# Performance work log

Measured on AMD Instinct MI355X. Metric: run time of the kernel, lower is better.

Reference implementation:

```python
import jax, jax.numpy as jnp
import numpy as np

DIM = 512
HEADS = 8
DIM_HEAD = 64
SCALE = DIM_HEAD ** -0.5


def setup_inputs() -> dict:
    key = jax.random.key(0)
    ks = jax.random.split(key, 4)
    b, n = 4, 2048
    x = jax.random.normal(ks[0], (b, n, DIM), dtype=jnp.float32)
    Wq = jax.random.normal(ks[1], (DIM, HEADS * DIM_HEAD), dtype=jnp.float32) * (DIM ** -0.5)
    Wkv = jax.random.normal(ks[2], (DIM, 2 * HEADS * DIM_HEAD), dtype=jnp.float32) * (DIM ** -0.5)
    Wo = jax.random.normal(ks[3], (HEADS * DIM_HEAD, DIM), dtype=jnp.float32) * ((HEADS * DIM_HEAD) ** -0.5)
    bo = jnp.zeros((DIM,), dtype=jnp.float32)
    return {"x": x, "Wq": Wq, "Wkv": Wkv, "Wo": Wo, "bo": bo}


def reference(x, Wq, Wkv, Wo, bo):
    b, n, _ = x.shape
    # context = x (self-attention path, kv_include_self=False)
    q = x @ Wq                      # [b, n, h*d]
    kv = x @ Wkv                    # [b, n, 2*h*d]
    k, v = jnp.split(kv, 2, axis=-1)

    def split_heads(t):
        return t.reshape(b, n, HEADS, DIM_HEAD).transpose(0, 2, 1, 3)  # [b,h,n,d]

    q, k, v = split_heads(q), split_heads(k), split_heads(v)
    dots = jnp.einsum('bhid,bhjd->bhij', q, k) * SCALE  # [b,h,n,n]
    attn = jax.nn.softmax(dots, axis=-1)
    out = jnp.einsum('bhij,bhjd->bhid', attn, v)        # [b,h,n,d]
    out = out.transpose(0, 2, 1, 3).reshape(b, n, HEADS * DIM_HEAD)
    return out @ Wo + bo
```

## Files before the change

### kernel.cpp

```cpp
#include <hip/hip_runtime.h>
#include <hip/hip_bf16.h>

typedef short bf16x8 __attribute__((ext_vector_type(8)));
typedef float fx4    __attribute__((ext_vector_type(4)));

#if __has_builtin(__builtin_amdgcn_exp2f)
#define EXP2 __builtin_amdgcn_exp2f
#else
#define EXP2 exp2f
#endif

__device__ __forceinline__ unsigned pk2(float a, float b) {
  union { __hip_bfloat162 h; unsigned u; } cv;
  cv.h = __float22bfloat162_rn(float2{a, b});
  return cv.u;
}
__device__ __forceinline__ uint2 pk4(const fx4& v) {
  uint2 r;
  r.x = pk2(v[0], v[1]);
  r.y = pk2(v[2], v[3]);
  return r;
}

__device__ __forceinline__ void gld16(const void* g, void* l) {
  __builtin_amdgcn_global_load_lds(
      (const __attribute__((address_space(1))) unsigned int*)g,
      (__attribute__((address_space(3))) unsigned int*)l, 16, 0, 0);
}

__device__ __forceinline__ void bar_raw() {
  asm volatile("s_barrier" ::: "memory");
}
__device__ __forceinline__ void bar_lgkm() {
  asm volatile("s_waitcnt lgkmcnt(0)\ns_barrier" ::: "memory");
}
__device__ __forceinline__ void bar_lgkm_vm4() {
  asm volatile("s_waitcnt vmcnt(4) lgkmcnt(0)\ns_barrier" ::: "memory");
}
__device__ __forceinline__ void cfence() { asm volatile("" ::: "memory"); }

__global__ __launch_bounds__(256) void prep_kernel(
    const float* __restrict__ x, const float* __restrict__ Wq,
    const float* __restrict__ Wkv, const float* __restrict__ Wo,
    short* __restrict__ xb, short* __restrict__ WallT, short* __restrict__ WoT,
    float qscale) {
  const int bx = blockIdx.x, tid = threadIdx.x;
  if (bx < 4096) {
    int i = bx * 256 + tid;
    const float4 s = *(const float4*)(x + (size_t)i * 4);
    uint2 o; o.x = pk2(s.x, s.y); o.y = pk2(s.z, s.w);
    *(uint2*)(xb + (size_t)i * 4) = o;
    return;
  }
  __shared__ float t[32][33];
  const int idx = bx - 4096;
  const int wb = idx & 63, kt = (idx >> 6) * 32;
  const bool mode0 = wb < 48;
  const int ct = (mode0 ? wb : wb - 48) * 32;
  const int tx = tid & 31, ty = tid >> 5;
  short* outT = mode0 ? WallT : WoT;
#pragma unroll
  for (int s = 0; s < 4; ++s) {
    int k = kt + ty + s * 8;
    int c = ct + tx;
    float v;
    if (mode0) v = (c < 512) ? Wq[(size_t)k * 512 + c] * qscale
                             : Wkv[(size_t)k * 1024 + (c - 512)];
    else       v = Wo[(size_t)k * 512 + c];
    t[ty + s * 8][tx] = v;
  }
  __syncthreads();
#pragma unroll
  for (int s = 0; s < 4; ++s) {
    int c = ct + ty + s * 8;
    int k = kt + tx;
    unsigned u = __float_as_uint(t[tx][ty + s * 8]);
    u = (u + 0x7fffu + ((u >> 16) & 1u)) >> 16;
    outT[(size_t)c * 512 + k] = (short)u;
  }
}

__global__ __launch_bounds__(256) void gemm_qkv(
    const short* __restrict__ A, const short* __restrict__ Bt,
    short* __restrict__ oq, short* __restrict__ ok, short* __restrict__ ovT) {
  __shared__ short As[2 * 128 * 32];
  __shared__ short Bs[2 * 128 * 32];
  const int K = 512;
  const int tid = threadIdx.x;
  const int wave = tid >> 6, lane = tid & 63;
  const int quad = lane >> 4, l15 = lane & 15;
  const int wm = wave >> 1, wn = wave & 1;
  const int m0 = blockIdx.y * 128, n0 = blockIdx.x * 128;
  const bool swapped = (n0 < 1024);

  int arow[4], aoff[4];
#pragma unroll
  for (int c = 0; c < 4; ++c) {
    int u = c * 256 + tid;
    int slab = u >> 9, r2 = u & 511;
    arow[c] = r2 >> 2;
    aoff[c] = slab * 32 + (r2 & 3) * 8;
  }

  fx4 acc[4][4];
#pragma unroll
  for (int i = 0; i < 4; ++i)
#pragma unroll
    for (int j = 0; j < 4; ++j) acc[i][j] = fx4{0.f, 0.f, 0.f, 0.f};

  bf16x8 apre[4];
#pragma unroll
  for (int c = 0; c < 4; ++c)
    apre[c] = *(const bf16x8*)(A + (size_t)(m0 + arow[c]) * K + aoff[c]);

  for (int k0 = 0; k0 < K; k0 += 64) {
    bar_raw();
#pragma unroll
    for (int c = 0; c < 4; ++c)
      *(bf16x8*)(As + (size_t)(c * 256 + tid) * 8) = apre[c];
#pragma unroll
    for (int c = 0; c < 4; ++c) {
      int u = c * 256 + tid;
      int slab = u >> 9, r2 = u & 511;
      gld16(Bt + (size_t)(n0 + (r2 >> 2)) * K + k0 + slab * 32 + (r2 & 3) * 8,
            Bs + (size_t)(c * 256 + wave * 64) * 8);
    }
    cfence();
    {
      int kn = (k0 + 64) & 511;
#pragma unroll
      for (int c = 0; c < 4; ++c)
        apre[c] = *(const bf16x8*)(A + (size_t)(m0 + arow[c]) * K + kn + aoff[c]);
    }
    bar_lgkm_vm4();

#pragma unroll
    for (int ks2 = 0; ks2 < 2; ++ks2) {
      bf16x8 af[4], bfr[4];
#pragma unroll
      for (int i = 0; i < 4; ++i)
        af[i] = *(const bf16x8*)(As + ks2 * 4096 + (wm * 64 + i * 16 + l15) * 32 + quad * 8);
#pragma unroll
      for (int i = 0; i < 4; ++i)
        bfr[i] = *(const bf16x8*)(Bs + ks2 * 4096 + (wn * 64 + i * 16 + l15) * 32 + quad * 8);
      if (swapped) {
#pragma unroll
        for (int mi = 0; mi < 4; ++mi)
#pragma unroll
          for (int ni = 0; ni < 4; ++ni)
            acc[mi][ni] = __builtin_amdgcn_mfma_f32_16x16x32_bf16(bfr[ni], af[mi], acc[mi][ni], 0, 0, 0);
      } else {
#pragma unroll
        for (int mi = 0; mi < 4; ++mi)
#pragma unroll
          for (int ni = 0; ni < 4; ++ni)
            acc[mi][ni] = __builtin_amdgcn_mfma_f32_16x16x32_bf16(af[mi], bfr[ni], acc[mi][ni], 0, 0, 0);
      }
    }
  }

  const int rowb = m0 + wm * 64;
  const int colb = n0 + wn * 64;
  const int cls = n0 >> 9;
  if (cls < 2) {
    short* base = (cls == 0) ? oq : ok;
#pragma unroll
    for (int mi = 0; mi < 4; ++mi) {
      int t = rowb + mi * 16 + l15;
      int bb = t >> 11, ii = t & 2047;
#pragma unroll
      for (int ni = 0; ni < 4; ++ni) {
        int f = (colb + ni * 16 + quad * 4) & 511;
        int hh = f >> 6, dd = f & 63;
        *(uint2*)(base + ((size_t)(bb * 8 + hh) * 2048 + ii) * 64 + dd) = pk4(acc[mi][ni]);
      }
    }
  } else {
#pragma unroll
    for (int mi = 0; mi < 4; ++mi) {
      int rbase = rowb + mi * 16 + quad * 4;
      int bb = rbase >> 11;
      int ii = rbase & 2047;
#pragma unroll
      for (int ni = 0; ni < 4; ++ni) {
        int c = (colb + ni * 16 + l15) & 511;
        int hh = c >> 6, dd = c & 63;
        *(uint2*)(ovT + ((size_t)(bb * 8 + hh) * 64 + dd) * 2048 + ii) = pk4(acc[mi][ni]);
      }
    }
  }
}

__global__ __launch_bounds__(256) void gemm_out(
    const short* __restrict__ A, const short* __restrict__ Bt,
    float* __restrict__ of, const float* __restrict__ bias) {
  __shared__ short As[2 * 64 * 32];
  __shared__ short Bs[2 * 128 * 32];
  const int K = 512, N = 512;
  const int tid = threadIdx.x;
  const int wave = tid >> 6, lane = tid & 63;
  const int quad = lane >> 4, l15 = lane & 15;
  const int wm = wave >> 1, wn = wave & 1;
  const int m0 = blockIdx.y * 64, n0 = blockIdx.x * 128;

  int arow[2], aoff[2], brow[4], boff[4];
#pragma unroll
  for (int c = 0; c < 2; ++c) {
    int u = c * 256 + tid;
    int slab = u >> 8, r2 = u & 255;
    arow[c] = r2 >> 2; aoff[c] = slab * 32 + (r2 & 3) * 8;
  }
#pragma unroll
  for (int c = 0; c < 4; ++c) {
    int u = c * 256 + tid;
    int slab = u >> 9, r2 = u & 511;
    brow[c] = r2 >> 2; boff[c] = slab * 32 + (r2 & 3) * 8;
  }

  fx4 acc[2][4];
#pragma unroll
  for (int i = 0; i < 2; ++i)
#pragma unroll
    for (int j = 0; j < 4; ++j) acc[i][j] = fx4{0.f, 0.f, 0.f, 0.f};

  bf16x8 apre[2], bpre[4];
#pragma unroll
  for (int c = 0; c < 2; ++c)
    apre[c] = *(const bf16x8*)(A + (size_t)(m0 + arow[c]) * K + aoff[c]);
#pragma unroll
  for (int c = 0; c < 4; ++c)
    bpre[c] = *(const bf16x8*)(Bt + (size_t)(n0 + brow[c]) * K + boff[c]);

  for (int k0 = 0; k0 < K; k0 += 64) {
    bar_raw();
#pragma unroll
    for (int c = 0; c < 2; ++c)
      *(bf16x8*)(As + (size_t)(c * 256 + tid) * 8) = apre[c];
#pragma unroll
    for (int c = 0; c < 4; ++c)
      *(bf16x8*)(Bs + (size_t)(c * 256 + tid) * 8) = bpre[c];
    {
      int kn = (k0 + 64) & 511;
#pragma unroll
      for (int c = 0; c < 2; ++c)
        apre[c] = *(const bf16x8*)(A + (size_t)(m0 + arow[c]) * K + kn + aoff[c]);
#pragma unroll
      for (int c = 0; c < 4; ++c)
        bpre[c] = *(const bf16x8*)(Bt + (size_t)(n0 + brow[c]) * K + kn + boff[c]);
    }
    bar_lgkm();

#pragma unroll
    for (int ks2 = 0; ks2 < 2; ++ks2) {
      bf16x8 af[2], bfr[4];
#pragma unroll
      for (int i = 0; i < 2; ++i)
        af[i] = *(const bf16x8*)(As + ks2 * 2048 + (wm * 32 + i * 16 + l15) * 32 + quad * 8);
#pragma unroll
      for (int i = 0; i < 4; ++i)
        bfr[i] = *(const bf16x8*)(Bs + ks2 * 4096 + (wn * 64 + i * 16 + l15) * 32 + quad * 8);
#pragma unroll
      for (int mi = 0; mi < 2; ++mi)
#pragma unroll
        for (int ni = 0; ni < 4; ++ni)
          acc[mi][ni] = __builtin_amdgcn_mfma_f32_16x16x32_bf16(af[mi], bfr[ni], acc[mi][ni], 0, 0, 0);
    }
  }

  const int rowb = m0 + wm * 32;
  const int colb = n0 + wn * 64;
#pragma unroll
  for (int mi = 0; mi < 2; ++mi)
#pragma unroll
    for (int ni = 0; ni < 4; ++ni) {
      int cg = colb + ni * 16 + l15;
      float bv = bias[cg];
#pragma unroll
      for (int r = 0; r < 4; ++r) {
        int rg = rowb + mi * 16 + quad * 4 + r;
        of[(size_t)rg * N + cg] = acc[mi][ni][r] + bv;
      }
    }
}

__global__ __launch_bounds__(256) void attn_kernel(
    const short* __restrict__ Q, const short* __restrict__ K,
    const short* __restrict__ Vt, short* __restrict__ O) {
  __shared__ short Ks[64 * 64];
  __shared__ short Vs[64 * 64];
  __shared__ short Ps[4 * 32 * 72];

  const int tid = threadIdx.x;
  const int wave = tid >> 6, lane = tid & 63;
  const int quad = lane >> 4, l15 = lane & 15;
  const int bh = blockIdx.y;
  const int b = bh >> 3, h = bh & 7;
  const int i0 = blockIdx.x * 128 + wave * 32;
  short* Pw = Ps + wave * (32 * 72);

  const int idx0 = tid, idx1 = 256 + tid;
  const int row0 = idx0 >> 3, sg0 = (idx0 & 7) ^ (row0 & 7);
  const int row1 = idx1 >> 3, sg1 = (idx1 & 7) ^ (row1 & 7);
  const short* Kb = K + (size_t)bh * 2048 * 64;
  const short* Vb = Vt + (size_t)bh * 64 * 2048;

  bf16x8 qf[2][2];
#pragma unroll
  for (int it = 0; it < 2; ++it)
#pragma unroll
    for (int ks = 0; ks < 2; ++ks)
      qf[it][ks] = *(const bf16x8*)(Q + ((size_t)bh * 2048 + i0 + it * 16 + l15) * 64 + ks * 32 + quad * 8);

  bf16x8 ones;
#pragma unroll
  for (int c = 0; c < 8; ++c) ones[c] = (short)0x3F80;

  fx4 oacc[2][4];
  fx4 acc_l[2] = { fx4{0.f,0.f,0.f,0.f}, fx4{0.f,0.f,0.f,0.f} };
#pragma unroll
  for (int it = 0; it < 2; ++it)
#pragma unroll
    for (int dt = 0; dt < 4; ++dt) oacc[it][dt] = fx4{0.f, 0.f, 0.f, 0.f};

  bf16x8 kpre0, kpre1, vpre0, vpre1;
  kpre0 = *(const bf16x8*)(Kb + (size_t)row0 * 64 + sg0 * 8);
  kpre1 = *(const bf16x8*)(Kb + (size_t)row1 * 64 + sg1 * 8);
  vpre0 = *(const bf16x8*)(Vb + (size_t)row0 * 2048 + sg0 * 8);
  vpre1 = *(const bf16x8*)(Vb + (size_t)row1 * 2048 + sg1 * 8);

  for (int j0 = 0; j0 < 2048; j0 += 64) {
    bar_raw();
    *(bf16x8*)(Ks + idx0 * 8) = kpre0;
    *(bf16x8*)(Ks + idx1 * 8) = kpre1;
    *(bf16x8*)(Vs + idx0 * 8) = vpre0;
    *(bf16x8*)(Vs + idx1 * 8) = vpre1;
    cfence();
    {
      int jn = (j0 + 64) & 2047;
      kpre0 = *(const bf16x8*)(Kb + (size_t)(jn + row0) * 64 + sg0 * 8);
      kpre1 = *(const bf16x8*)(Kb + (size_t)(jn + row1) * 64 + sg1 * 8);
      vpre0 = *(const bf16x8*)(Vb + (size_t)row0 * 2048 + jn + sg0 * 8);
      vpre1 = *(const bf16x8*)(Vb + (size_t)row1 * 2048 + jn + sg1 * 8);
    }
    bar_lgkm();

    fx4 s[2][4];
#pragma unroll
    for (int it = 0; it < 2; ++it)
#pragma unroll
      for (int jt = 0; jt < 4; ++jt) s[it][jt] = fx4{0.f, 0.f, 0.f, 0.f};
#pragma unroll
    for (int ks = 0; ks < 2; ++ks) {
#pragma unroll
      for (int jt = 0; jt < 4; ++jt) {
        bf16x8 kf = *(const bf16x8*)(Ks + (jt * 16 + l15) * 64 + (((ks * 4 + quad) ^ (l15 & 7)) * 8));
#pragma unroll
        for (int it = 0; it < 2; ++it)
          s[it][jt] = __builtin_amdgcn_mfma_f32_16x16x32_bf16(kf, qf[it][ks], s[it][jt], 0, 0, 0);
      }
    }

#pragma unroll
    for (int it = 0; it < 2; ++it)
#pragma unroll
      for (int jt = 0; jt < 4; ++jt) {
#pragma unroll
        for (int r = 0; r < 4; ++r) s[it][jt][r] = EXP2(s[it][jt][r]);
        *(uint2*)(Pw + (it * 16 + l15) * 72 + jt * 16 + quad * 4) = pk4(s[it][jt]);
      }

#pragma unroll
    for (int kj = 0; kj < 2; ++kj) {
      bf16x8 pf[2];
#pragma unroll
      for (int it = 0; it < 2; ++it) {
        pf[it] = *(const bf16x8*)(Pw + (it * 16 + l15) * 72 + kj * 32 + quad * 8);
        acc_l[it] = __builtin_amdgcn_mfma_f32_16x16x32_bf16(ones, pf[it], acc_l[it], 0, 0, 0);
      }
#pragma unroll
      for (int dt = 0; dt < 4; ++dt) {
        bf16x8 vf = *(const bf16x8*)(Vs + (dt * 16 + l15) * 64 + (((kj * 4 + quad) ^ (l15 & 7)) * 8));
#pragma unroll
        for (int it = 0; it < 2; ++it)
          oacc[it][dt] = __builtin_amdgcn_mfma_f32_16x16x32_bf16(vf, pf[it], oacc[it][dt], 0, 0, 0);
      }
    }
  }

#pragma unroll
  for (int it = 0; it < 2; ++it) {
    float inv = __builtin_amdgcn_rcpf(acc_l[it][0]);
    size_t rowbase = ((size_t)b * 2048 + i0 + it * 16 + l15) * 512 + h * 64;
#pragma unroll
    for (int dt = 0; dt < 4; ++dt) {
      fx4 o = oacc[it][dt] * inv;
      *(uint2*)(O + rowbase + dt * 16 + quad * 4) = pk4(o);
    }
  }
}

extern "C" void kernel_launch(void* const* d_in, const int* in_sizes, int n_in,
                              void* d_out, int out_size, void* d_ws, size_t ws_size,
                              hipStream_t stream) {
  const float* x   = (const float*)d_in[0];
  const float* Wq  = (const float*)d_in[1];
  const float* Wkv = (const float*)d_in[2];
  const float* Wo  = (const float*)d_in[3];
  const float* bo  = (const float*)d_in[4];
  float* out = (float*)d_out;

  char* p = (char*)d_ws;
  short* xb    = (short*)p; p += (size_t)8192 * 512 * 2;
  short* WallT = (short*)p; p += (size_t)1536 * 512 * 2;
  short* WoT   = (short*)p; p += (size_t)512 * 512 * 2;
  short* qb    = (short*)p; p += (size_t)32 * 2048 * 64 * 2;
  short* kb    = (short*)p; p += (size_t)32 * 2048 * 64 * 2;
  short* vTb   = (short*)p; p += (size_t)32 * 64 * 2048 * 2;
  short* Ob    = (short*)p; p += (size_t)8192 * 512 * 2;

  const float qscale = 0.125f * 1.4426950408889634f;

  prep_kernel<<<5120, 256, 0, stream>>>(x, Wq, Wkv, Wo, xb, WallT, WoT, qscale);
  gemm_qkv<<<dim3(12, 64), 256, 0, stream>>>(xb, WallT, qb, kb, vTb);
  attn_kernel<<<dim3(16, 32), 256, 0, stream>>>(qb, kb, vTb, Ob);
  gemm_out<<<dim3(4, 128), 256, 0, stream>>>(Ob, WoT, out, bo);
}
```

Baseline: 164.9 us.

## Fuse x bf16 conversion into QKV GEMM and keep P in registers

The separate pass that converts x to bf16 is removed; the QKV GEMM now loads fp32 x directly and packs it to bf16 while staging into LDS, which drops a full write and re-read of the activation. In attention, the exp'd scores are packed into registers and fed to 16x16x16 MFMAs directly, which removes the per-tile LDS round trip for P. The row sums now come from VALU adds plus cross-lane shuffles instead of a ones-matrix MFMA. In exchange, the GEMM reads twice as many bytes of A per tile and uses more prefetch registers, and the attention kernel uses the smaller-K MFMA shape.

```diff
diff --git a/kernel.cpp b/kernel.cpp
--- a/kernel.cpp
+++ b/kernel.cpp
@@ -2,6 +2,7 @@
 #include <hip/hip_bf16.h>
 
 typedef short bf16x8 __attribute__((ext_vector_type(8)));
+typedef short bf16x4 __attribute__((ext_vector_type(4)));
 typedef float fx4    __attribute__((ext_vector_type(4)));
 
 #if __has_builtin(__builtin_amdgcn_exp2f)
@@ -21,6 +22,11 @@
   r.y = pk2(v[2], v[3]);
   return r;
 }
+__device__ __forceinline__ bf16x4 pk4b(const fx4& v) {
+  union { uint2 u; bf16x4 b; } c;
+  c.u = pk4(v);
+  return c.b;
+}
 
 __device__ __forceinline__ void gld16(const void* g, void* l) {
   __builtin_amdgcn_global_load_lds(
@@ -34,26 +40,18 @@
 __device__ __forceinline__ void bar_lgkm() {
   asm volatile("s_waitcnt lgkmcnt(0)\ns_barrier" ::: "memory");
 }
-__device__ __forceinline__ void bar_lgkm_vm4() {
-  asm volatile("s_waitcnt vmcnt(4) lgkmcnt(0)\ns_barrier" ::: "memory");
+__device__ __forceinline__ void bar_lgkm_vm8() {
+  asm volatile("s_waitcnt vmcnt(8) lgkmcnt(0)\ns_barrier" ::: "memory");
 }
 __device__ __forceinline__ void cfence() { asm volatile("" ::: "memory"); }
 
 __global__ __launch_bounds__(256) void prep_kernel(
-    const float* __restrict__ x, const float* __restrict__ Wq,
-    const float* __restrict__ Wkv, const float* __restrict__ Wo,
-    short* __restrict__ xb, short* __restrict__ WallT, short* __restrict__ WoT,
-    float qscale) {
-  const int bx = blockIdx.x, tid = threadIdx.x;
-  if (bx < 4096) {
-    int i = bx * 256 + tid;
-    const float4 s = *(const float4*)(x + (size_t)i * 4);
-    uint2 o; o.x = pk2(s.x, s.y); o.y = pk2(s.z, s.w);
-    *(uint2*)(xb + (size_t)i * 4) = o;
-    return;
-  }
+    const float* __restrict__ Wq, const float* __restrict__ Wkv,
+    const float* __restrict__ Wo,
+    short* __restrict__ WallT, short* __restrict__ WoT, float qscale) {
   __shared__ float t[32][33];
-  const int idx = bx - 4096;
+  const int tid = threadIdx.x;
+  const int idx = blockIdx.x;
   const int wb = idx & 63, kt = (idx >> 6) * 32;
   const bool mode0 = wb < 48;
   const int ct = (mode0 ? wb : wb - 48) * 32;
@@ -81,7 +79,7 @@
 }
 
 __global__ __launch_bounds__(256) void gemm_qkv(
-    const short* __restrict__ A, const short* __restrict__ Bt,
+    const float* __restrict__ A, const short* __restrict__ Bt,
     short* __restrict__ oq, short* __restrict__ ok, short* __restrict__ ovT) {
   __shared__ short As[2 * 128 * 32];
   __shared__ short Bs[2 * 128 * 32];
@@ -108,16 +106,25 @@
 #pragma unroll
     for (int j = 0; j < 4; ++j) acc[i][j] = fx4{0.f, 0.f, 0.f, 0.f};
 
-  bf16x8 apre[4];
-#pragma unroll
-  for (int c = 0; c < 4; ++c)
-    apre[c] = *(const bf16x8*)(A + (size_t)(m0 + arow[c]) * K + aoff[c]);
+  float4 apre[8];
+#pragma unroll
+  for (int c = 0; c < 4; ++c) {
+    const float* base = A + (size_t)(m0 + arow[c]) * K + aoff[c];
+    apre[2 * c]     = *(const float4*)(base);
+    apre[2 * c + 1] = *(const float4*)(base + 4);
+  }
 
   for (int k0 = 0; k0 < K; k0 += 64) {
     bar_raw();
 #pragma unroll
-    for (int c = 0; c < 4; ++c)
-      *(bf16x8*)(As + (size_t)(c * 256 + tid) * 8) = apre[c];
+    for (int c = 0; c < 4; ++c) {
+      uint4 w;
+      w.x = pk2(apre[2 * c].x, apre[2 * c].y);
+      w.y = pk2(apre[2 * c].z, apre[2 * c].w);
+      w.z = pk2(apre[2 * c + 1].x, apre[2 * c + 1].y);
+      w.w = pk2(apre[2 * c + 1].z, apre[2 * c + 1].w);
+      *(uint4*)(As + (size_t)(c * 256 + tid) * 8) = w;
+    }
 #pragma unroll
     for (int c = 0; c < 4; ++c) {
       int u = c * 256 + tid;
@@ -129,10 +136,13 @@
     {
       int kn = (k0 + 64) & 511;
 #pragma unroll
-      for (int c = 0; c < 4; ++c)
-        apre[c] = *(const bf16x8*)(A + (size_t)(m0 + arow[c]) * K + kn + aoff[c]);
-    }
-    bar_lgkm_vm4();
+      for (int c = 0; c < 4; ++c) {
+        const float* base = A + (size_t)(m0 + arow[c]) * K + kn + aoff[c];
+        apre[2 * c]     = *(const float4*)(base);
+        apre[2 * c + 1] = *(const float4*)(base + 4);
+      }
+    }
+    bar_lgkm_vm8();
 
 #pragma unroll
     for (int ks2 = 0; ks2 < 2; ++ks2) {
@@ -288,7 +298,6 @@
     const short* __restrict__ Vt, short* __restrict__ O) {
   __shared__ short Ks[64 * 64];
   __shared__ short Vs[64 * 64];
-  __shared__ short Ps[4 * 32 * 72];
 
   const int tid = threadIdx.x;
   const int wave = tid >> 6, lane = tid & 63;
@@ -296,7 +305,6 @@
   const int bh = blockIdx.y;
   const int b = bh >> 3, h = bh & 7;
   const int i0 = blockIdx.x * 128 + wave * 32;
-  short* Pw = Ps + wave * (32 * 72);
 
   const int idx0 = tid, idx1 = 256 + tid;
   const int row0 = idx0 >> 3, sg0 = (idx0 & 7) ^ (row0 & 7);
@@ -311,12 +319,8 @@
     for (int ks = 0; ks < 2; ++ks)
       qf[it][ks] = *(const bf16x8*)(Q + ((size_t)bh * 2048 + i0 + it * 16 + l15) * 64 + ks * 32 + quad * 8);
 
-  bf16x8 ones;
-#pragma unroll
-  for (int c = 0; c < 8; ++c) ones[c] = (short)0x3F80;
-
   fx4 oacc[2][4];
-  fx4 acc_l[2] = { fx4{0.f,0.f,0.f,0.f}, fx4{0.f,0.f,0.f,0.f} };
+  fx4 lacc[2] = { fx4{0.f,0.f,0.f,0.f}, fx4{0.f,0.f,0.f,0.f} };
 #pragma unroll
   for (int it = 0; it < 2; ++it)
 #pragma unroll
@@ -360,36 +364,37 @@
       }
     }
 
-#pragma unroll
-    for (int it = 0; it < 2; ++it)
+    bf16x4 pp[2][4];
+#pragma unroll
+    for (int it = 0; it < 2; ++it) {
 #pragma unroll
       for (int jt = 0; jt < 4; ++jt) {
 #pragma unroll
         for (int r = 0; r < 4; ++r) s[it][jt][r] = EXP2(s[it][jt][r]);
-        *(uint2*)(Pw + (it * 16 + l15) * 72 + jt * 16 + quad * 4) = pk4(s[it][jt]);
-      }
-
-#pragma unroll
-    for (int kj = 0; kj < 2; ++kj) {
-      bf16x8 pf[2];
-#pragma unroll
-      for (int it = 0; it < 2; ++it) {
-        pf[it] = *(const bf16x8*)(Pw + (it * 16 + l15) * 72 + kj * 32 + quad * 8);
-        acc_l[it] = __builtin_amdgcn_mfma_f32_16x16x32_bf16(ones, pf[it], acc_l[it], 0, 0, 0);
-      }
+        pp[it][jt] = pk4b(s[it][jt]);
+      }
+      lacc[it] += (s[it][0] + s[it][1]) + (s[it][2] + s[it][3]);
+    }
+
+#pragma unroll
+    for (int kc = 0; kc < 4; ++kc) {
 #pragma unroll
       for (int dt = 0; dt < 4; ++dt) {
-        bf16x8 vf = *(const bf16x8*)(Vs + (dt * 16 + l15) * 64 + (((kj * 4 + quad) ^ (l15 & 7)) * 8));
+        int seg = (kc * 2 + (quad >> 1)) ^ (l15 & 7);
+        bf16x4 av = *(const bf16x4*)(Vs + (dt * 16 + l15) * 64 + seg * 8 + (quad & 1) * 4);
 #pragma unroll
         for (int it = 0; it < 2; ++it)
-          oacc[it][dt] = __builtin_amdgcn_mfma_f32_16x16x32_bf16(vf, pf[it], oacc[it][dt], 0, 0, 0);
+          oacc[it][dt] = __builtin_amdgcn_mfma_f32_16x16x16bf16_1k(av, pp[it][kc], oacc[it][dt], 0, 0, 0);
       }
     }
   }
 
 #pragma unroll
   for (int it = 0; it < 2; ++it) {
-    float inv = __builtin_amdgcn_rcpf(acc_l[it][0]);
+    float l_s = (lacc[it][0] + lacc[it][1]) + (lacc[it][2] + lacc[it][3]);
+    l_s += __shfl_xor(l_s, 16);
+    l_s += __shfl_xor(l_s, 32);
+    float inv = __builtin_amdgcn_rcpf(l_s);
     size_t rowbase = ((size_t)b * 2048 + i0 + it * 16 + l15) * 512 + h * 64;
 #pragma unroll
     for (int dt = 0; dt < 4; ++dt) {
@@ -410,7 +415,6 @@
   float* out = (float*)d_out;
 
   char* p = (char*)d_ws;
-  short* xb    = (short*)p; p += (size_t)8192 * 512 * 2;
   short* WallT = (short*)p; p += (size_t)1536 * 512 * 2;
   short* WoT   = (short*)p; p += (size_t)512 * 512 * 2;
   short* qb    = (short*)p; p += (size_t)32 * 2048 * 64 * 2;
@@ -420,8 +424,8 @@
 
   const float qscale = 0.125f * 1.4426950408889634f;
 
-  prep_kernel<<<5120, 256, 0, stream>>>(x, Wq, Wkv, Wo, xb, WallT, WoT, qscale);
-  gemm_qkv<<<dim3(12, 64), 256, 0, stream>>>(xb, WallT, qb, kb, vTb);
+  prep_kernel<<<1024, 256, 0, stream>>>(Wq, Wkv, Wo, WallT, WoT, qscale);
+  gemm_qkv<<<dim3(12, 64), 256, 0, stream>>>(x, WallT, qb, kb, vTb);
   attn_kernel<<<dim3(16, 32), 256, 0, stream>>>(qb, kb, vTb, Ob);
   gemm_out<<<dim3(4, 128), 256, 0, stream>>>(Ob, WoT, out, bo);
 }
```

Result: slower. 176.3 us (+6.9%).

## Load K/V fragments directly from global into registers, drop LDS staging

Applied to the files above, without the earlier changes.

Removes the shared-memory K and V tiles and their per-iteration barriers. Each wave now reads its MFMA K and V fragments straight from global memory into registers, with K prefetched one tile ahead. The softmax denominator is accumulated in fp32 with VALU adds and cross-lane shuffles instead of an MFMA against a vector of ones. The cost is that each of the four waves fetches the same K/V data separately, which quadruples global/L2 traffic, and V is loaded without a prefetch, so its latency is exposed.

```diff
diff --git a/kernel.cpp b/kernel.cpp
--- a/kernel.cpp
+++ b/kernel.cpp
@@ -286,8 +286,6 @@
 __global__ __launch_bounds__(256) void attn_kernel(
     const short* __restrict__ Q, const short* __restrict__ K,
     const short* __restrict__ Vt, short* __restrict__ O) {
-  __shared__ short Ks[64 * 64];
-  __shared__ short Vs[64 * 64];
   __shared__ short Ps[4 * 32 * 72];
 
   const int tid = threadIdx.x;
@@ -298,9 +296,6 @@
   const int i0 = blockIdx.x * 128 + wave * 32;
   short* Pw = Ps + wave * (32 * 72);
 
-  const int idx0 = tid, idx1 = 256 + tid;
-  const int row0 = idx0 >> 3, sg0 = (idx0 & 7) ^ (row0 & 7);
-  const int row1 = idx1 >> 3, sg1 = (idx1 & 7) ^ (row1 & 7);
   const short* Kb = K + (size_t)bh * 2048 * 64;
   const short* Vb = Vt + (size_t)bh * 64 * 2048;
 
@@ -311,38 +306,27 @@
     for (int ks = 0; ks < 2; ++ks)
       qf[it][ks] = *(const bf16x8*)(Q + ((size_t)bh * 2048 + i0 + it * 16 + l15) * 64 + ks * 32 + quad * 8);
 
-  bf16x8 ones;
-#pragma unroll
-  for (int c = 0; c < 8; ++c) ones[c] = (short)0x3F80;
-
   fx4 oacc[2][4];
-  fx4 acc_l[2] = { fx4{0.f,0.f,0.f,0.f}, fx4{0.f,0.f,0.f,0.f} };
+  fx4 lacc[2] = { fx4{0.f,0.f,0.f,0.f}, fx4{0.f,0.f,0.f,0.f} };
 #pragma unroll
   for (int it = 0; it < 2; ++it)
 #pragma unroll
     for (int dt = 0; dt < 4; ++dt) oacc[it][dt] = fx4{0.f, 0.f, 0.f, 0.f};
 
-  bf16x8 kpre0, kpre1, vpre0, vpre1;
-  kpre0 = *(const bf16x8*)(Kb + (size_t)row0 * 64 + sg0 * 8);
-  kpre1 = *(const bf16x8*)(Kb + (size_t)row1 * 64 + sg1 * 8);
-  vpre0 = *(const bf16x8*)(Vb + (size_t)row0 * 2048 + sg0 * 8);
-  vpre1 = *(const bf16x8*)(Vb + (size_t)row1 * 2048 + sg1 * 8);
+  bf16x8 kf[8];
+#pragma unroll
+  for (int ks = 0; ks < 2; ++ks)
+#pragma unroll
+    for (int jt = 0; jt < 4; ++jt)
+      kf[ks * 4 + jt] = *(const bf16x8*)(Kb + (size_t)(jt * 16 + l15) * 64 + ks * 32 + quad * 8);
 
   for (int j0 = 0; j0 < 2048; j0 += 64) {
-    bar_raw();
-    *(bf16x8*)(Ks + idx0 * 8) = kpre0;
-    *(bf16x8*)(Ks + idx1 * 8) = kpre1;
-    *(bf16x8*)(Vs + idx0 * 8) = vpre0;
-    *(bf16x8*)(Vs + idx1 * 8) = vpre1;
-    cfence();
-    {
-      int jn = (j0 + 64) & 2047;
-      kpre0 = *(const bf16x8*)(Kb + (size_t)(jn + row0) * 64 + sg0 * 8);
-      kpre1 = *(const bf16x8*)(Kb + (size_t)(jn + row1) * 64 + sg1 * 8);
-      vpre0 = *(const bf16x8*)(Vb + (size_t)row0 * 2048 + jn + sg0 * 8);
-      vpre1 = *(const bf16x8*)(Vb + (size_t)row1 * 2048 + jn + sg1 * 8);
-    }
-    bar_lgkm();
+    bf16x8 vf[8];
+#pragma unroll
+    for (int kj = 0; kj < 2; ++kj)
+#pragma unroll
+      for (int dt = 0; dt < 4; ++dt)
+        vf[kj * 4 + dt] = *(const bf16x8*)(Vb + (size_t)(dt * 16 + l15) * 2048 + j0 + kj * 32 + quad * 8);
 
     fx4 s[2][4];
 #pragma unroll
@@ -350,46 +334,53 @@
 #pragma unroll
       for (int jt = 0; jt < 4; ++jt) s[it][jt] = fx4{0.f, 0.f, 0.f, 0.f};
 #pragma unroll
-    for (int ks = 0; ks < 2; ++ks) {
-#pragma unroll
-      for (int jt = 0; jt < 4; ++jt) {
-        bf16x8 kf = *(const bf16x8*)(Ks + (jt * 16 + l15) * 64 + (((ks * 4 + quad) ^ (l15 & 7)) * 8));
+    for (int ks = 0; ks < 2; ++ks)
+#pragma unroll
+      for (int jt = 0; jt < 4; ++jt)
 #pragma unroll
         for (int it = 0; it < 2; ++it)
-          s[it][jt] = __builtin_amdgcn_mfma_f32_16x16x32_bf16(kf, qf[it][ks], s[it][jt], 0, 0, 0);
-      }
-    }
-
-#pragma unroll
-    for (int it = 0; it < 2; ++it)
+          s[it][jt] = __builtin_amdgcn_mfma_f32_16x16x32_bf16(kf[ks * 4 + jt], qf[it][ks], s[it][jt], 0, 0, 0);
+
+#pragma unroll
+    for (int it = 0; it < 2; ++it) {
 #pragma unroll
       for (int jt = 0; jt < 4; ++jt) {
 #pragma unroll
         for (int r = 0; r < 4; ++r) s[it][jt][r] = EXP2(s[it][jt][r]);
         *(uint2*)(Pw + (it * 16 + l15) * 72 + jt * 16 + quad * 4) = pk4(s[it][jt]);
       }
+      lacc[it] += (s[it][0] + s[it][1]) + (s[it][2] + s[it][3]);
+    }
+
+    {
+      int jn = (j0 + 64) & 2047;
+#pragma unroll
+      for (int ks = 0; ks < 2; ++ks)
+#pragma unroll
+        for (int jt = 0; jt < 4; ++jt)
+          kf[ks * 4 + jt] = *(const bf16x8*)(Kb + (size_t)(jn + jt * 16 + l15) * 64 + ks * 32 + quad * 8);
+    }
 
 #pragma unroll
     for (int kj = 0; kj < 2; ++kj) {
       bf16x8 pf[2];
 #pragma unroll
-      for (int it = 0; it < 2; ++it) {
+      for (int it = 0; it < 2; ++it)
         pf[it] = *(const bf16x8*)(Pw + (it * 16 + l15) * 72 + kj * 32 + quad * 8);
-        acc_l[it] = __builtin_amdgcn_mfma_f32_16x16x32_bf16(ones, pf[it], acc_l[it], 0, 0, 0);
-      }
-#pragma unroll
-      for (int dt = 0; dt < 4; ++dt) {
-        bf16x8 vf = *(const bf16x8*)(Vs + (dt * 16 + l15) * 64 + (((kj * 4 + quad) ^ (l15 & 7)) * 8));
+#pragma unroll
+      for (int dt = 0; dt < 4; ++dt)
 #pragma unroll
         for (int it = 0; it < 2; ++it)
-          oacc[it][dt] = __builtin_amdgcn_mfma_f32_16x16x32_bf16(vf, pf[it], oacc[it][dt], 0, 0, 0);
-      }
+          oacc[it][dt] = __builtin_amdgcn_mfma_f32_16x16x32_bf16(vf[kj * 4 + dt], pf[it], oacc[it][dt], 0, 0, 0);
     }
   }
 
 #pragma unroll
   for (int it = 0; it < 2; ++it) {
-    float inv = __builtin_amdgcn_rcpf(acc_l[it][0]);
+    float l_s = (lacc[it][0] + lacc[it][1]) + (lacc[it][2] + lacc[it][3]);
+    l_s += __shfl_xor(l_s, 16);
+    l_s += __shfl_xor(l_s, 32);
+    float inv = __builtin_amdgcn_rcpf(l_s);
     size_t rowbase = ((size_t)b * 2048 + i0 + it * 16 + l15) * 512 + h * 64;
 #pragma unroll
     for (int dt = 0; dt < 4; ++dt) {
```

After: 231.9 us. +40.6%, slower.

## Shrink GEMM and attention tiles, reorder grid, compute softmax denominator with VALU

Applied to the files above, without the earlier changes.

Both GEMMs move to narrower N tiles (QKV 128x64, output 64x64), and the grid is transposed so blockIdx.x walks M. The attention kernel drops to 2 waves and 64 query rows per block, which doubles the block count. Each thread now stages 4 chunks of K and V instead of 2. The softmax row sum, previously an MFMA against a ones vector, becomes a VALU accumulation followed by cross-lane shuffles, removing MFMAs from the inner loop. More blocks should give better occupancy and CU coverage on MI355X, but each block gets less operand reuse and each loaded K/V tile feeds fewer query rows.

```diff
diff --git a/kernel.cpp b/kernel.cpp
--- a/kernel.cpp
+++ b/kernel.cpp
@@ -84,13 +84,13 @@
     const short* __restrict__ A, const short* __restrict__ Bt,
     short* __restrict__ oq, short* __restrict__ ok, short* __restrict__ ovT) {
   __shared__ short As[2 * 128 * 32];
-  __shared__ short Bs[2 * 128 * 32];
+  __shared__ short Bs[2 * 64 * 32];
   const int K = 512;
   const int tid = threadIdx.x;
   const int wave = tid >> 6, lane = tid & 63;
   const int quad = lane >> 4, l15 = lane & 15;
   const int wm = wave >> 1, wn = wave & 1;
-  const int m0 = blockIdx.y * 128, n0 = blockIdx.x * 128;
+  const int m0 = blockIdx.x * 128, n0 = blockIdx.y * 64;
   const bool swapped = (n0 < 1024);
 
   int arow[4], aoff[4];
@@ -102,11 +102,11 @@
     aoff[c] = slab * 32 + (r2 & 3) * 8;
   }
 
-  fx4 acc[4][4];
+  fx4 acc[4][2];
 #pragma unroll
   for (int i = 0; i < 4; ++i)
 #pragma unroll
-    for (int j = 0; j < 4; ++j) acc[i][j] = fx4{0.f, 0.f, 0.f, 0.f};
+    for (int j = 0; j < 2; ++j) acc[i][j] = fx4{0.f, 0.f, 0.f, 0.f};
 
   bf16x8 apre[4];
 #pragma unroll
@@ -119,9 +119,9 @@
     for (int c = 0; c < 4; ++c)
       *(bf16x8*)(As + (size_t)(c * 256 + tid) * 8) = apre[c];
 #pragma unroll
-    for (int c = 0; c < 4; ++c) {
+    for (int c = 0; c < 2; ++c) {
       int u = c * 256 + tid;
-      int slab = u >> 9, r2 = u & 511;
+      int slab = u >> 8, r2 = u & 255;
       gld16(Bt + (size_t)(n0 + (r2 >> 2)) * K + k0 + slab * 32 + (r2 & 3) * 8,
             Bs + (size_t)(c * 256 + wave * 64) * 8);
     }
@@ -136,31 +136,31 @@
 
 #pragma unroll
     for (int ks2 = 0; ks2 < 2; ++ks2) {
-      bf16x8 af[4], bfr[4];
+      bf16x8 af[4], bfr[2];
 #pragma unroll
       for (int i = 0; i < 4; ++i)
         af[i] = *(const bf16x8*)(As + ks2 * 4096 + (wm * 64 + i * 16 + l15) * 32 + quad * 8);
 #pragma unroll
-      for (int i = 0; i < 4; ++i)
-        bfr[i] = *(const bf16x8*)(Bs + ks2 * 4096 + (wn * 64 + i * 16 + l15) * 32 + quad * 8);
+      for (int i = 0; i < 2; ++i)
+        bfr[i] = *(const bf16x8*)(Bs + ks2 * 2048 + (wn * 32 + i * 16 + l15) * 32 + quad * 8);
       if (swapped) {
 #pragma unroll
         for (int mi = 0; mi < 4; ++mi)
 #pragma unroll
-          for (int ni = 0; ni < 4; ++ni)
+          for (int ni = 0; ni < 2; ++ni)
             acc[mi][ni] = __builtin_amdgcn_mfma_f32_16x16x32_bf16(bfr[ni], af[mi], acc[mi][ni], 0, 0, 0);
       } else {
 #pragma unroll
         for (int mi = 0; mi < 4; ++mi)
 #pragma unroll
-          for (int ni = 0; ni < 4; ++ni)
+          for (int ni = 0; ni < 2; ++ni)
             acc[mi][ni] = __builtin_amdgcn_mfma_f32_16x16x32_bf16(af[mi], bfr[ni], acc[mi][ni], 0, 0, 0);
       }
     }
   }
 
   const int rowb = m0 + wm * 64;
-  const int colb = n0 + wn * 64;
+  const int colb = n0 + wn * 32;
   const int cls = n0 >> 9;
   if (cls < 2) {
     short* base = (cls == 0) ? oq : ok;
@@ -169,7 +169,7 @@
       int t = rowb + mi * 16 + l15;
       int bb = t >> 11, ii = t & 2047;
 #pragma unroll
-      for (int ni = 0; ni < 4; ++ni) {
+      for (int ni = 0; ni < 2; ++ni) {
         int f = (colb + ni * 16 + quad * 4) & 511;
         int hh = f >> 6, dd = f & 63;
         *(uint2*)(base + ((size_t)(bb * 8 + hh) * 2048 + ii) * 64 + dd) = pk4(acc[mi][ni]);
@@ -182,7 +182,7 @@
       int bb = rbase >> 11;
       int ii = rbase & 2047;
 #pragma unroll
-      for (int ni = 0; ni < 4; ++ni) {
+      for (int ni = 0; ni < 2; ++ni) {
         int c = (colb + ni * 16 + l15) & 511;
         int hh = c >> 6, dd = c & 63;
         *(uint2*)(ovT + ((size_t)(bb * 8 + hh) * 64 + dd) * 2048 + ii) = pk4(acc[mi][ni]);
@@ -195,84 +195,75 @@
     const short* __restrict__ A, const short* __restrict__ Bt,
     float* __restrict__ of, const float* __restrict__ bias) {
   __shared__ short As[2 * 64 * 32];
-  __shared__ short Bs[2 * 128 * 32];
+  __shared__ short Bs[2 * 64 * 32];
   const int K = 512, N = 512;
   const int tid = threadIdx.x;
   const int wave = tid >> 6, lane = tid & 63;
   const int quad = lane >> 4, l15 = lane & 15;
   const int wm = wave >> 1, wn = wave & 1;
-  const int m0 = blockIdx.y * 64, n0 = blockIdx.x * 128;
-
-  int arow[2], aoff[2], brow[4], boff[4];
+  const int m0 = blockIdx.x * 64, n0 = blockIdx.y * 64;
+
+  int arow[2], aoff[2], brow[2], boff[2];
 #pragma unroll
   for (int c = 0; c < 2; ++c) {
     int u = c * 256 + tid;
     int slab = u >> 8, r2 = u & 255;
     arow[c] = r2 >> 2; aoff[c] = slab * 32 + (r2 & 3) * 8;
-  }
-#pragma unroll
-  for (int c = 0; c < 4; ++c) {
-    int u = c * 256 + tid;
-    int slab = u >> 9, r2 = u & 511;
-    brow[c] = r2 >> 2; boff[c] = slab * 32 + (r2 & 3) * 8;
-  }
-
-  fx4 acc[2][4];
+    brow[c] = arow[c]; boff[c] = aoff[c];
+  }
+
+  fx4 acc[2][2];
 #pragma unroll
   for (int i = 0; i < 2; ++i)
 #pragma unroll
-    for (int j = 0; j < 4; ++j) acc[i][j] = fx4{0.f, 0.f, 0.f, 0.f};
-
-  bf16x8 apre[2], bpre[4];
-#pragma unroll
-  for (int c = 0; c < 2; ++c)
+    for (int j = 0; j < 2; ++j) acc[i][j] = fx4{0.f, 0.f, 0.f, 0.f};
+
+  bf16x8 apre[2], bpre[2];
+#pragma unroll
+  for (int c = 0; c < 2; ++c) {
     apre[c] = *(const bf16x8*)(A + (size_t)(m0 + arow[c]) * K + aoff[c]);
-#pragma unroll
-  for (int c = 0; c < 4; ++c)
     bpre[c] = *(const bf16x8*)(Bt + (size_t)(n0 + brow[c]) * K + boff[c]);
+  }
 
   for (int k0 = 0; k0 < K; k0 += 64) {
     bar_raw();
 #pragma unroll
-    for (int c = 0; c < 2; ++c)
+    for (int c = 0; c < 2; ++c) {
       *(bf16x8*)(As + (size_t)(c * 256 + tid) * 8) = apre[c];
-#pragma unroll
-    for (int c = 0; c < 4; ++c)
       *(bf16x8*)(Bs + (size_t)(c * 256 + tid) * 8) = bpre[c];
+    }
     {
       int kn = (k0 + 64) & 511;
 #pragma unroll
-      for (int c = 0; c < 2; ++c)
+      for (int c = 0; c < 2; ++c) {
         apre[c] = *(const bf16x8*)(A + (size_t)(m0 + arow[c]) * K + kn + aoff[c]);
-#pragma unroll
-      for (int c = 0; c < 4; ++c)
         bpre[c] = *(const bf16x8*)(Bt + (size_t)(n0 + brow[c]) * K + kn + boff[c]);
+      }
     }
     bar_lgkm();
 
 #pragma unroll
     for (int ks2 = 0; ks2 < 2; ++ks2) {
-      bf16x8 af[2], bfr[4];
-#pragma unroll
-      for (int i = 0; i < 2; ++i)
-        af[i] = *(const bf16x8*)(As + ks2 * 2048 + (wm * 32 + i * 16 + l15) * 32 + quad * 8);
-#pragma unroll
-      for (int i = 0; i < 4; ++i)
-        bfr[i] = *(const bf16x8*)(Bs + ks2 * 4096 + (wn * 64 + i * 16 + l15) * 32 + quad * 8);
+      bf16x8 af[2], bfr[2];
+#pragma unroll
+      for (int i = 0; i < 2; ++i) {
+        af[i]  = *(const bf16x8*)(As + ks2 * 2048 + (wm * 32 + i * 16 + l15) * 32 + quad * 8);
+        bfr[i] = *(const bf16x8*)(Bs + ks2 * 2048 + (wn * 32 + i * 16 + l15) * 32 + quad * 8);
+      }
 #pragma unroll
       for (int mi = 0; mi < 2; ++mi)
 #pragma unroll
-        for (int ni = 0; ni < 4; ++ni)
+        for (int ni = 0; ni < 2; ++ni)
           acc[mi][ni] = __builtin_amdgcn_mfma_f32_16x16x32_bf16(af[mi], bfr[ni], acc[mi][ni], 0, 0, 0);
     }
   }
 
   const int rowb = m0 + wm * 32;
-  const int colb = n0 + wn * 64;
+  const int colb = n0 + wn * 32;
 #pragma unroll
   for (int mi = 0; mi < 2; ++mi)
 #pragma unroll
-    for (int ni = 0; ni < 4; ++ni) {
+    for (int ni = 0; ni < 2; ++ni) {
       int cg = colb + ni * 16 + l15;
       float bv = bias[cg];
 #pragma unroll
@@ -283,24 +274,28 @@
     }
 }
 
-__global__ __launch_bounds__(256) void attn_kernel(
+__global__ __launch_bounds__(128) void attn_kernel(
     const short* __restrict__ Q, const short* __restrict__ K,
     const short* __restrict__ Vt, short* __restrict__ O) {
   __shared__ short Ks[64 * 64];
   __shared__ short Vs[64 * 64];
-  __shared__ short Ps[4 * 32 * 72];
+  __shared__ short Ps[2 * 32 * 72];
 
   const int tid = threadIdx.x;
   const int wave = tid >> 6, lane = tid & 63;
   const int quad = lane >> 4, l15 = lane & 15;
   const int bh = blockIdx.y;
   const int b = bh >> 3, h = bh & 7;
-  const int i0 = blockIdx.x * 128 + wave * 32;
+  const int i0 = blockIdx.x * 64 + wave * 32;
   short* Pw = Ps + wave * (32 * 72);
 
-  const int idx0 = tid, idx1 = 256 + tid;
-  const int row0 = idx0 >> 3, sg0 = (idx0 & 7) ^ (row0 & 7);
-  const int row1 = idx1 >> 3, sg1 = (idx1 & 7) ^ (row1 & 7);
+  int srow[4], ssg[4];
+#pragma unroll
+  for (int c = 0; c < 4; ++c) {
+    int u = c * 128 + tid;
+    srow[c] = u >> 3;
+    ssg[c] = (u & 7) ^ (srow[c] & 7);
+  }
   const short* Kb = K + (size_t)bh * 2048 * 64;
   const short* Vb = Vt + (size_t)bh * 64 * 2048;
 
@@ -311,36 +306,35 @@
     for (int ks = 0; ks < 2; ++ks)
       qf[it][ks] = *(const bf16x8*)(Q + ((size_t)bh * 2048 + i0 + it * 16 + l15) * 64 + ks * 32 + quad * 8);
 
-  bf16x8 ones;
-#pragma unroll
-  for (int c = 0; c < 8; ++c) ones[c] = (short)0x3F80;
-
   fx4 oacc[2][4];
-  fx4 acc_l[2] = { fx4{0.f,0.f,0.f,0.f}, fx4{0.f,0.f,0.f,0.f} };
+  fx4 lacc[2] = { fx4{0.f,0.f,0.f,0.f}, fx4{0.f,0.f,0.f,0.f} };
 #pragma unroll
   for (int it = 0; it < 2; ++it)
 #pragma unroll
     for (int dt = 0; dt < 4; ++dt) oacc[it][dt] = fx4{0.f, 0.f, 0.f, 0.f};
 
-  bf16x8 kpre0, kpre1, vpre0, vpre1;
-  kpre0 = *(const bf16x8*)(Kb + (size_t)row0 * 64 + sg0 * 8);
-  kpre1 = *(const bf16x8*)(Kb + (size_t)row1 * 64 + sg1 * 8);
-  vpre0 = *(const bf16x8*)(Vb + (size_t)row0 * 2048 + sg0 * 8);
-  vpre1 = *(const bf16x8*)(Vb + (size_t)row1 * 2048 + sg1 * 8);
+  bf16x8 kpre[4], vpre[4];
+#pragma unroll
+  for (int c = 0; c < 4; ++c) {
+    kpre[c] = *(const bf16x8*)(Kb + (size_t)srow[c] * 64 + ssg[c] * 8);
+    vpre[c] = *(const bf16x8*)(Vb + (size_t)srow[c] * 2048 + ssg[c] * 8);
+  }
 
   for (int j0 = 0; j0 < 2048; j0 += 64) {
     bar_raw();
-    *(bf16x8*)(Ks + idx0 * 8) = kpre0;
-    *(bf16x8*)(Ks + idx1 * 8) = kpre1;
-    *(bf16x8*)(Vs + idx0 * 8) = vpre0;
-    *(bf16x8*)(Vs + idx1 * 8) = vpre1;
+#pragma unroll
+    for (int c = 0; c < 4; ++c) {
+      *(bf16x8*)(Ks + (size_t)(c * 128 + tid) * 8) = kpre[c];
+      *(bf16x8*)(Vs + (size_t)(c * 128 + tid) * 8) = vpre[c];
+    }
     cfence();
     {
       int jn = (j0 + 64) & 2047;
-      kpre0 = *(const bf16x8*)(Kb + (size_t)(jn + row0) * 64 + sg0 * 8);
-      kpre1 = *(const bf16x8*)(Kb + (size_t)(jn + row1) * 64 + sg1 * 8);
-      vpre0 = *(const bf16x8*)(Vb + (size_t)row0 * 2048 + jn + sg0 * 8);
-      vpre1 = *(const bf16x8*)(Vb + (size_t)row1 * 2048 + jn + sg1 * 8);
+#pragma unroll
+      for (int c = 0; c < 4; ++c) {
+        kpre[c] = *(const bf16x8*)(Kb + (size_t)(jn + srow[c]) * 64 + ssg[c] * 8);
+        vpre[c] = *(const bf16x8*)(Vb + (size_t)srow[c] * 2048 + jn + ssg[c] * 8);
+      }
     }
     bar_lgkm();
 
@@ -361,22 +355,22 @@
     }
 
 #pragma unroll
-    for (int it = 0; it < 2; ++it)
+    for (int it = 0; it < 2; ++it) {
 #pragma unroll
       for (int jt = 0; jt < 4; ++jt) {
 #pragma unroll
         for (int r = 0; r < 4; ++r) s[it][jt][r] = EXP2(s[it][jt][r]);
         *(uint2*)(Pw + (it * 16 + l15) * 72 + jt * 16 + quad * 4) = pk4(s[it][jt]);
       }
+      lacc[it] += (s[it][0] + s[it][1]) + (s[it][2] + s[it][3]);
+    }
 
 #pragma unroll
     for (int kj = 0; kj < 2; ++kj) {
       bf16x8 pf[2];
 #pragma unroll
-      for (int it = 0; it < 2; ++it) {
+      for (int it = 0; it < 2; ++it)
         pf[it] = *(const bf16x8*)(Pw + (it * 16 + l15) * 72 + kj * 32 + quad * 8);
-        acc_l[it] = __builtin_amdgcn_mfma_f32_16x16x32_bf16(ones, pf[it], acc_l[it], 0, 0, 0);
-      }
 #pragma unroll
       for (int dt = 0; dt < 4; ++dt) {
         bf16x8 vf = *(const bf16x8*)(Vs + (dt * 16 + l15) * 64 + (((kj * 4 + quad) ^ (l15 & 7)) * 8));
@@ -389,7 +383,10 @@
 
 #pragma unroll
   for (int it = 0; it < 2; ++it) {
-    float inv = __builtin_amdgcn_rcpf(acc_l[it][0]);
+    float l_s = (lacc[it][0] + lacc[it][1]) + (lacc[it][2] + lacc[it][3]);
+    l_s += __shfl_xor(l_s, 16);
+    l_s += __shfl_xor(l_s, 32);
+    float inv = __builtin_amdgcn_rcpf(l_s);
     size_t rowbase = ((size_t)b * 2048 + i0 + it * 16 + l15) * 512 + h * 64;
 #pragma unroll
     for (int dt = 0; dt < 4; ++dt) {
@@ -421,7 +418,7 @@
   const float qscale = 0.125f * 1.4426950408889634f;
 
   prep_kernel<<<5120, 256, 0, stream>>>(x, Wq, Wkv, Wo, xb, WallT, WoT, qscale);
-  gemm_qkv<<<dim3(12, 64), 256, 0, stream>>>(xb, WallT, qb, kb, vTb);
-  attn_kernel<<<dim3(16, 32), 256, 0, stream>>>(qb, kb, vTb, Ob);
-  gemm_out<<<dim3(4, 128), 256, 0, stream>>>(Ob, WoT, out, bo);
-}
+  gemm_qkv<<<dim3(64, 24), 256, 0, stream>>>(xb, WallT, qb, kb, vTb);
+  attn_kernel<<<dim3(32, 32), 128, 0, stream>>>(qb, kb, vTb, Ob);
+  gemm_out<<<dim3(128, 8), 256, 0, stream>>>(Ob, WoT, out, bo);
+}
```

Result: slower. 170.8 us (+3.6%).
